# Kernel optimization log

Hardware: AMD Instinct MI355X
Metric: run time of the kernel (lower is better)

Reference implementation:

```python
import jax, jax.numpy as jnp
import numpy as np

B, L, CIN, COUT, HEADS = 8, 2048, 256, 256, 4
HD = COUT // HEADS
NEG_SLOPE = 0.2


def setup_inputs() -> dict:
    key = jax.random.key(0)
    k1, k2, k3, k4, k5 = jax.random.split(key, 5)
    x = jax.random.normal(k1, (B, L, CIN), dtype=jnp.float32)
    adj_mask = jax.random.randint(k2, (B, L, L), 0, 2) > 0  # bool [B,L,L]
    W = jax.random.normal(k3, (COUT, CIN), dtype=jnp.float32) * (1.0 / np.sqrt(CIN))
    att_src = jax.random.normal(k4, (1, HEADS, 1, HD), dtype=jnp.float32) * 0.1
    att_dst = jax.random.normal(k5, (1, HEADS, 1, HD), dtype=jnp.float32) * 0.1
    return {"x": x, "adj_mask": adj_mask, "W": W, "att_src": att_src, "att_dst": att_dst}


def reference(x, adj_mask, W, att_src, att_dst):
    Bb, Ll, _ = x.shape
    # linear projection (no bias), split heads: [B, H, L, D]
    h = jnp.einsum('blc,oc->blo', x, W).reshape(Bb, Ll, HEADS, HD).transpose(0, 2, 1, 3)
    # additive GAT scores
    a_src = jnp.sum(h * att_src, axis=-1, keepdims=True)          # [B,H,L,1]
    a_dst = jnp.sum(h * att_dst, axis=-1, keepdims=True)          # [B,H,L,1]
    e = a_src + jnp.swapaxes(a_dst, 2, 3)                          # [B,H,L,L]
    e = jnp.where(e >= 0, e, NEG_SLOPE * e)                        # leaky relu
    fill = jnp.finfo(e.dtype).min
    e = jnp.where(adj_mask[:, None, :, :], e, fill)                # mask non-edges
    alpha = jax.nn.softmax(e, axis=-1)                             # [B,H,L,L]
    # dropout is identity in eval/reference mode
    out = jnp.einsum('bhij,bhjd->bhid', alpha, h)                  # [B,H,L,D]
    return out.transpose(0, 2, 1, 3).reshape(Bb, Ll, COUT)
```

## Files before the change

### kernel.cpp

```cpp
#include <hip/hip_runtime.h>

#define B_ 8
#define L_ 2048
#define CIN_ 256
#define COUT_ 256
#define HEADS_ 4
#define HD_ 64
#define NEG_SLOPE_ 0.2f

#define TI 32
#define TJ 64

typedef __attribute__((ext_vector_type(4))) float f32x4;
typedef __attribute__((ext_vector_type(8))) __bf16 bf16x8;
typedef __attribute__((ext_vector_type(4))) __bf16 bf16x4;


__global__ __launch_bounds__(256, 2)
void proj_kernel(const float* __restrict__ x, const float* __restrict__ W,
                 const float* __restrict__ att_src, const float* __restrict__ att_dst,
                 __bf16* __restrict__ hT, float* __restrict__ a_src,
                 float* __restrict__ a_dst) {
  __shared__ __align__(16) __bf16 Wl[COUT_][80];
  __shared__ __align__(16) __bf16 Al[2][2][512];
  __shared__ __align__(16) __bf16 Tl[4][64][48];

  const int tid = threadIdx.x;
  const int r0 = blockIdx.x * TI;
  const int b  = r0 >> 11;
  const int l0 = r0 & (L_ - 1);

  const int w = tid >> 6, lane = tid & 63, col = lane & 15, q = lane >> 4;
  const int si = tid >> 3, soct = tid & 7;
  const int wn = tid >> 2, wkq = tid & 3;

  f32x4 acc[2][4];
#pragma unroll
  for (int mt = 0; mt < 2; ++mt)
#pragma unroll
    for (int nt = 0; nt < 4; ++nt) acc[mt][nt] = (f32x4)0.f;

  for (int kc = 0; kc < CIN_ / 64; ++kc) {
    __syncthreads();
#pragma unroll
    for (int rg = 0; rg < 4; ++rg) {
      const int row = rg * 64 + wn;
      const float4* ws = (const float4*)(W + (size_t)row * CIN_ + kc * 64 + wkq * 16);
#pragma unroll
      for (int u = 0; u < 4; ++u) {
        float4 f = ws[u];
        bf16x4 v;
        v[0] = (__bf16)f.x; v[1] = (__bf16)f.y; v[2] = (__bf16)f.z; v[3] = (__bf16)f.w;
        *(bf16x4*)&Wl[row][wkq * 16 + u * 4] = v;
      }
    }
    {
      const float4* xs = (const float4*)(x + (size_t)(r0 + si) * CIN_ + kc * 64 + soct * 8);
      float4 f0 = xs[0], f1 = xs[1];
      bf16x8 v;
      v[0] = (__bf16)f0.x; v[1] = (__bf16)f0.y; v[2] = (__bf16)f0.z; v[3] = (__bf16)f0.w;
      v[4] = (__bf16)f1.x; v[5] = (__bf16)f1.y; v[6] = (__bf16)f1.z; v[7] = (__bf16)f1.w;
      *(bf16x8*)&Al[si >> 4][soct >> 2][(((soct & 3) << 4) + (si & 15)) << 3] = v;
    }
    __syncthreads();

    bf16x8 af[2][2], bfr[2][4];
#pragma unroll
    for (int mt = 0; mt < 2; ++mt)
#pragma unroll
      for (int kt = 0; kt < 2; ++kt)
        af[mt][kt] = *(const bf16x8*)&Al[mt][kt][lane << 3];
#pragma unroll
    for (int kt = 0; kt < 2; ++kt)
#pragma unroll
      for (int nt = 0; nt < 4; ++nt)
        bfr[kt][nt] = *(const bf16x8*)&Wl[w * 64 + nt * 16 + col][kt * 32 + q * 8];
#pragma unroll
    for (int kt = 0; kt < 2; ++kt)
#pragma unroll
      for (int mt = 0; mt < 2; ++mt)
#pragma unroll
        for (int nt = 0; nt < 4; ++nt)
          acc[mt][nt] = __builtin_amdgcn_mfma_f32_16x16x32_bf16(
              af[mt][kt], bfr[kt][nt], acc[mt][nt], 0, 0, 0);
  }

  float asv[4], adv[4];
#pragma unroll
  for (int nt = 0; nt < 4; ++nt) {
    asv[nt] = att_src[w * 64 + nt * 16 + col];
    adv[nt] = att_dst[w * 64 + nt * 16 + col];
  }
#pragma unroll
  for (int mt = 0; mt < 2; ++mt)
#pragma unroll
    for (int reg = 0; reg < 4; ++reg) {
      float s = 0.f, d = 0.f;
#pragma unroll
      for (int nt = 0; nt < 4; ++nt) {
        s = fmaf(acc[mt][nt][reg], asv[nt], s);
        d = fmaf(acc[mt][nt][reg], adv[nt], d);
      }
      s += __shfl_xor(s, 1, 64); d += __shfl_xor(d, 1, 64);
      s += __shfl_xor(s, 2, 64); d += __shfl_xor(d, 2, 64);
      s += __shfl_xor(s, 4, 64); d += __shfl_xor(d, 4, 64);
      s += __shfl_xor(s, 8, 64); d += __shfl_xor(d, 8, 64);
      if (col == 0) {
        int il = mt * 16 + q * 4 + reg;
        a_src[((size_t)(b * HEADS_ + w) << 11) + l0 + il] = s;
        a_dst[((size_t)(b * HEADS_ + w) << 11) + l0 + il] = d;
      }
    }

#pragma unroll
  for (int mt = 0; mt < 2; ++mt)
#pragma unroll
    for (int nt = 0; nt < 4; ++nt)
#pragma unroll
      for (int reg = 0; reg < 4; ++reg)
        Tl[w][nt * 16 + col][mt * 16 + q * 4 + reg] = (__bf16)acc[mt][nt][reg];
  __syncthreads();
  {
    const size_t hrow = ((size_t)(b * COUT_ + w * 64 + lane) << 11) + l0;
#pragma unroll
    for (int u = 0; u < 4; ++u) {
      uint4 v = *(const uint4*)&Tl[w][lane][u * 8];
      *(uint4*)(hT + hrow + u * 8) = v;
    }
  }
}

__global__ __launch_bounds__(256, 2)
void attn_kernel(const __bf16* __restrict__ hT, const float* __restrict__ a_src,
                 const float* __restrict__ a_dst, const int* __restrict__ adj,
                 float* __restrict__ out) {
  __shared__ __align__(16) __bf16 Pf[HEADS_][2][2][512];
  __shared__ __align__(16) __bf16 hs[COUT_][80];
  __shared__ float l_s[HEADS_][TI];

  const int tid = threadIdx.x;
  const int b  = blockIdx.x >> 6;
  const int i0 = (blockIdx.x & 63) * TI;

  const int w = tid >> 6, lane = tid & 63, col = lane & 15, q = lane >> 4;
  const int ii1 = tid >> 3, oct = tid & 7;
  const int mtp = ii1 >> 4, ktp = oct >> 2;
  const int lanep = ((oct & 3) << 4) + (ii1 & 15);

  float asr[HEADS_];
#pragma unroll
  for (int h = 0; h < HEADS_; ++h)
    asr[h] = a_src[((size_t)(b * HEADS_ + h) << 11) + i0 + ii1];

  float lacc[HEADS_] = {0.f, 0.f, 0.f, 0.f};
  f32x4 acc[2][4];
#pragma unroll
  for (int mt = 0; mt < 2; ++mt)
#pragma unroll
    for (int nt = 0; nt < 4; ++nt) acc[mt][nt] = (f32x4)0.f;

  for (int jt = 0; jt < L_ / TJ; ++jt) {
    const int j0 = jt * TJ;
    __syncthreads();

#pragma unroll
    for (int p = 0; p < 8; ++p) {
      int c = p * 32 + (tid >> 3);
      int seg = tid & 7;
      uint4 v = *(const uint4*)(hT + (((size_t)(b * COUT_ + c)) << 11) + j0 + seg * 8);
      *(uint4*)&hs[c][seg * 8] = v;
    }

    const int4* ap =
        (const int4*)(adj + (size_t)b * L_ * L_ + (size_t)(i0 + ii1) * L_ + j0 + oct * 8);
    const int4 m0 = ap[0], m1 = ap[1];
    const int am[8] = {m0.x, m0.y, m0.z, m0.w, m1.x, m1.y, m1.z, m1.w};

#pragma unroll
    for (int h = 0; h < HEADS_; ++h) {
      const float* ad = a_dst + ((size_t)(b * HEADS_ + h) << 11) + j0 + oct * 8;
      const float4 d0 = *(const float4*)ad;
      const float4 d1 = *(const float4*)(ad + 4);
      const float dv[8] = {d0.x, d0.y, d0.z, d0.w, d1.x, d1.y, d1.z, d1.w};
      bf16x8 pv;
      float ls = 0.f;
#pragma unroll
      for (int e = 0; e < 8; ++e) {
        float s = asr[h] + dv[e];
        s = (s >= 0.f) ? s : NEG_SLOPE_ * s;
        float p = am[e] ? __expf(s) : 0.f;
        ls += p;
        pv[e] = (__bf16)p;
      }
      lacc[h] += ls;
      *(bf16x8*)&Pf[h][mtp][ktp][lanep << 3] = pv;
    }
    __syncthreads();

    bf16x8 af[2][2], bfr[2][4];
#pragma unroll
    for (int mt = 0; mt < 2; ++mt)
#pragma unroll
      for (int kt = 0; kt < 2; ++kt)
        af[mt][kt] = *(const bf16x8*)&Pf[w][mt][kt][lane << 3];
#pragma unroll
    for (int kt = 0; kt < 2; ++kt)
#pragma unroll
      for (int nt = 0; nt < 4; ++nt)
        bfr[kt][nt] = *(const bf16x8*)&hs[w * 64 + nt * 16 + col][kt * 32 + q * 8];
#pragma unroll
    for (int kt = 0; kt < 2; ++kt)
#pragma unroll
      for (int mt = 0; mt < 2; ++mt)
#pragma unroll
        for (int nt = 0; nt < 4; ++nt)
          acc[mt][nt] = __builtin_amdgcn_mfma_f32_16x16x32_bf16(
              af[mt][kt], bfr[kt][nt], acc[mt][nt], 0, 0, 0);
  }

#pragma unroll
  for (int h = 0; h < HEADS_; ++h) {
    float v = lacc[h];
    v += __shfl_xor(v, 1, 64);
    v += __shfl_xor(v, 2, 64);
    v += __shfl_xor(v, 4, 64);
    if (oct == 0) l_s[h][ii1] = v;
  }
  __syncthreads();

#pragma unroll
  for (int mt = 0; mt < 2; ++mt)
#pragma unroll
    for (int reg = 0; reg < 4; ++reg) {
      const int il = mt * 16 + q * 4 + reg;
      const float linv = 1.0f / l_s[w][il];
#pragma unroll
      for (int nt = 0; nt < 4; ++nt) {
        const int c = w * 64 + nt * 16 + col;
        out[((size_t)(b * L_ + i0 + il)) * COUT_ + c] = acc[mt][nt][reg] * linv;
      }
    }
}

extern "C" void kernel_launch(void* const* d_in, const int* in_sizes, int n_in,
                              void* d_out, int out_size, void* d_ws, size_t ws_size,
                              hipStream_t stream) {
  const float* x       = (const float*)d_in[0];
  const int*   adj     = (const int*)d_in[1];
  const float* W       = (const float*)d_in[2];
  const float* att_src = (const float*)d_in[3];
  const float* att_dst = (const float*)d_in[4];
  float* out = (float*)d_out;

  __bf16* hT   = (__bf16*)d_ws;
  float* a_src = (float*)((char*)d_ws + (size_t)B_ * COUT_ * L_ * 2);
  float* a_dst = a_src + (size_t)B_ * HEADS_ * L_;

  proj_kernel<<<(B_ * L_) / TI, 256, 0, stream>>>(x, W, att_src, att_dst, hT, a_src, a_dst);
  attn_kernel<<<B_ * (L_ / TI), 256, 0, stream>>>(hT, a_src, a_dst, adj, out);
}
```

Before: 305.8 us.

## Enlarge attention row tile, load h fragments directly, prefetch next tile

```diff
diff --git a/kernel.cpp b/kernel.cpp
--- a/kernel.cpp
+++ b/kernel.cpp
@@ -9,7 +9,9 @@
 #define NEG_SLOPE_ 0.2f
 
 #define TI 32
+#define ATI 64
 #define TJ 64
+#define NJT (L_ / TJ)
 
 typedef __attribute__((ext_vector_type(4))) float f32x4;
 typedef __attribute__((ext_vector_type(8))) __bf16 bf16x8;
@@ -130,28 +132,38 @@
   }
 }
 
-__global__ __launch_bounds__(256, 2)
+__device__ __forceinline__ int sw_chunk(int c) {
+  return c ^ (((c >> 4) & 3) << 1);
+}
+
+__global__ __launch_bounds__(512, 2)
 void attn_kernel(const __bf16* __restrict__ hT, const float* __restrict__ a_src,
                  const float* __restrict__ a_dst, const int* __restrict__ adj,
                  float* __restrict__ out) {
-  __shared__ __align__(16) __bf16 Pf[HEADS_][2][2][512];
-  __shared__ __align__(16) __bf16 hs[COUT_][80];
-  __shared__ float l_s[HEADS_][TI];
+  __shared__ __align__(16) __bf16 Pf[HEADS_][4][2][512];
+  __shared__ float l_s[HEADS_][ATI];
 
   const int tid = threadIdx.x;
-  const int b  = blockIdx.x >> 6;
-  const int i0 = (blockIdx.x & 63) * TI;
+  const int b  = blockIdx.x & 7;
+  const int i0 = (blockIdx.x >> 3) * ATI;
 
   const int w = tid >> 6, lane = tid & 63, col = lane & 15, q = lane >> 4;
+  const int hh = w >> 1;
+  const int mh = (w & 1) * 2;
   const int ii1 = tid >> 3, oct = tid & 7;
   const int mtp = ii1 >> 4, ktp = oct >> 2;
   const int lanep = ((oct & 3) << 4) + (ii1 & 15);
+  const int pchunk = sw_chunk(lanep) << 3;
 
   float asr[HEADS_];
 #pragma unroll
   for (int h = 0; h < HEADS_; ++h)
     asr[h] = a_src[((size_t)(b * HEADS_ + h) << 11) + i0 + ii1];
 
+  const int* adjrow = adj + (size_t)b * L_ * L_ + (size_t)(i0 + ii1) * L_ + oct * 8;
+  const float* adbase = a_dst + ((size_t)b * HEADS_ << 11) + oct * 8;
+  const __bf16* hbase = hT + ((size_t)(b * COUT_ + hh * 64) << 11);
+
   float lacc[HEADS_] = {0.f, 0.f, 0.f, 0.f};
   f32x4 acc[2][4];
 #pragma unroll
@@ -159,55 +171,64 @@
 #pragma unroll
     for (int nt = 0; nt < 4; ++nt) acc[mt][nt] = (f32x4)0.f;
 
-  for (int jt = 0; jt < L_ / TJ; ++jt) {
-    const int j0 = jt * TJ;
-    __syncthreads();
-
-#pragma unroll
-    for (int p = 0; p < 8; ++p) {
-      int c = p * 32 + (tid >> 3);
-      int seg = tid & 7;
-      uint4 v = *(const uint4*)(hT + (((size_t)(b * COUT_ + c)) << 11) + j0 + seg * 8);
-      *(uint4*)&hs[c][seg * 8] = v;
-    }
-
-    const int4* ap =
-        (const int4*)(adj + (size_t)b * L_ * L_ + (size_t)(i0 + ii1) * L_ + j0 + oct * 8);
-    const int4 m0 = ap[0], m1 = ap[1];
-    const int am[8] = {m0.x, m0.y, m0.z, m0.w, m1.x, m1.y, m1.z, m1.w};
-
+  int4 cadj0 = ((const int4*)adjrow)[0];
+  int4 cadj1 = ((const int4*)adjrow)[1];
+  float4 cad[HEADS_][2];
+#pragma unroll
+  for (int h = 0; h < HEADS_; ++h) {
+    cad[h][0] = *(const float4*)(adbase + ((size_t)h << 11));
+    cad[h][1] = *(const float4*)(adbase + ((size_t)h << 11) + 4);
+  }
+  bf16x8 bfr[2][4];
+#pragma unroll
+  for (int kt = 0; kt < 2; ++kt)
+#pragma unroll
+    for (int nt = 0; nt < 4; ++nt)
+      bfr[kt][nt] = *(const bf16x8*)(hbase + ((size_t)(nt * 16 + col) << 11) +
+                                     kt * 32 + q * 8);
+
+  for (int jt = 0; jt < NJT; ++jt) {
+    const int jn = (jt < NJT - 1) ? (jt + 1) * TJ : jt * TJ;
+
+    int4 nadj0 = ((const int4*)(adjrow + jn))[0];
+    int4 nadj1 = ((const int4*)(adjrow + jn))[1];
+
+    const int am[8] = {cadj0.x, cadj0.y, cadj0.z, cadj0.w,
+                       cadj1.x, cadj1.y, cadj1.z, cadj1.w};
+    bf16x8 pv[HEADS_];
 #pragma unroll
     for (int h = 0; h < HEADS_; ++h) {
-      const float* ad = a_dst + ((size_t)(b * HEADS_ + h) << 11) + j0 + oct * 8;
-      const float4 d0 = *(const float4*)ad;
-      const float4 d1 = *(const float4*)(ad + 4);
-      const float dv[8] = {d0.x, d0.y, d0.z, d0.w, d1.x, d1.y, d1.z, d1.w};
-      bf16x8 pv;
+      const float dv[8] = {cad[h][0].x, cad[h][0].y, cad[h][0].z, cad[h][0].w,
+                           cad[h][1].x, cad[h][1].y, cad[h][1].z, cad[h][1].w};
       float ls = 0.f;
 #pragma unroll
       for (int e = 0; e < 8; ++e) {
         float s = asr[h] + dv[e];
-        s = (s >= 0.f) ? s : NEG_SLOPE_ * s;
+        s = fmaxf(s, NEG_SLOPE_ * s);
         float p = am[e] ? __expf(s) : 0.f;
         ls += p;
-        pv[e] = (__bf16)p;
+        pv[h][e] = (__bf16)p;
       }
       lacc[h] += ls;
-      *(bf16x8*)&Pf[h][mtp][ktp][lanep << 3] = pv;
-    }
-    __syncthreads();
-
-    bf16x8 af[2][2], bfr[2][4];
+    }
+#pragma unroll
+    for (int h = 0; h < HEADS_; ++h) {
+      cad[h][0] = *(const float4*)(adbase + ((size_t)h << 11) + jn);
+      cad[h][1] = *(const float4*)(adbase + ((size_t)h << 11) + jn + 4);
+    }
+
+    __syncthreads();
+#pragma unroll
+    for (int h = 0; h < HEADS_; ++h)
+      *(bf16x8*)&Pf[h][mtp][ktp][pchunk] = pv[h];
+    __syncthreads();
+
+    bf16x8 af[2][2];
 #pragma unroll
     for (int mt = 0; mt < 2; ++mt)
 #pragma unroll
       for (int kt = 0; kt < 2; ++kt)
-        af[mt][kt] = *(const bf16x8*)&Pf[w][mt][kt][lane << 3];
-#pragma unroll
-    for (int kt = 0; kt < 2; ++kt)
-#pragma unroll
-      for (int nt = 0; nt < 4; ++nt)
-        bfr[kt][nt] = *(const bf16x8*)&hs[w * 64 + nt * 16 + col][kt * 32 + q * 8];
+        af[mt][kt] = *(const bf16x8*)&Pf[hh][mh + mt][kt][sw_chunk(lane) << 3];
 #pragma unroll
     for (int kt = 0; kt < 2; ++kt)
 #pragma unroll
@@ -216,6 +237,15 @@
         for (int nt = 0; nt < 4; ++nt)
           acc[mt][nt] = __builtin_amdgcn_mfma_f32_16x16x32_bf16(
               af[mt][kt], bfr[kt][nt], acc[mt][nt], 0, 0, 0);
+
+#pragma unroll
+    for (int kt = 0; kt < 2; ++kt)
+#pragma unroll
+      for (int nt = 0; nt < 4; ++nt)
+        bfr[kt][nt] = *(const bf16x8*)(hbase + ((size_t)(nt * 16 + col) << 11) +
+                                       jn + kt * 32 + q * 8);
+    cadj0 = nadj0;
+    cadj1 = nadj1;
   }
 
 #pragma unroll
@@ -232,11 +262,11 @@
   for (int mt = 0; mt < 2; ++mt)
 #pragma unroll
     for (int reg = 0; reg < 4; ++reg) {
-      const int il = mt * 16 + q * 4 + reg;
-      const float linv = 1.0f / l_s[w][il];
+      const int il = (mh + mt) * 16 + q * 4 + reg;
+      const float linv = 1.0f / l_s[hh][il];
 #pragma unroll
       for (int nt = 0; nt < 4; ++nt) {
-        const int c = w * 64 + nt * 16 + col;
+        const int c = hh * 64 + nt * 16 + col;
         out[((size_t)(b * L_ + i0 + il)) * COUT_ + c] = acc[mt][nt][reg] * linv;
       }
     }
@@ -257,5 +287,5 @@
   float* a_dst = a_src + (size_t)B_ * HEADS_ * L_;
 
   proj_kernel<<<(B_ * L_) / TI, 256, 0, stream>>>(x, W, att_src, att_dst, hT, a_src, a_dst);
-  attn_kernel<<<B_ * (L_ / TI), 256, 0, stream>>>(hT, a_src, a_dst, adj, out);
-}
+  attn_kernel<<<B_ * (L_ / ATI), 512, 0, stream>>>(hT, a_src, a_dst, adj, out);
+}
```

Result: faster. 280.6 us (-8.2%).

## Restructure attention kernel to register-direct MFMA operands without shared memory

Applied to the files above, without the earlier changes.

```diff
diff --git a/kernel.cpp b/kernel.cpp
--- a/kernel.cpp
+++ b/kernel.cpp
@@ -10,6 +10,7 @@
 
 #define TI 32
 #define TJ 64
+#define NJT (L_ / TJ)
 
 typedef __attribute__((ext_vector_type(4))) float f32x4;
 typedef __attribute__((ext_vector_type(8))) __bf16 bf16x8;
@@ -130,116 +131,102 @@
   }
 }
 
-__global__ __launch_bounds__(256, 2)
+__global__ __launch_bounds__(512, 4)
 void attn_kernel(const __bf16* __restrict__ hT, const float* __restrict__ a_src,
                  const float* __restrict__ a_dst, const int* __restrict__ adj,
                  float* __restrict__ out) {
-  __shared__ __align__(16) __bf16 Pf[HEADS_][2][2][512];
-  __shared__ __align__(16) __bf16 hs[COUT_][80];
-  __shared__ float l_s[HEADS_][TI];
-
   const int tid = threadIdx.x;
-  const int b  = blockIdx.x >> 6;
-  const int i0 = (blockIdx.x & 63) * TI;
+  const int b  = blockIdx.x & 7;
+  const int i0 = (blockIdx.x >> 3) * 32;
 
   const int w = tid >> 6, lane = tid & 63, col = lane & 15, q = lane >> 4;
-  const int ii1 = tid >> 3, oct = tid & 7;
-  const int mtp = ii1 >> 4, ktp = oct >> 2;
-  const int lanep = ((oct & 3) << 4) + (ii1 & 15);
-
-  float asr[HEADS_];
-#pragma unroll
-  for (int h = 0; h < HEADS_; ++h)
-    asr[h] = a_src[((size_t)(b * HEADS_ + h) << 11) + i0 + ii1];
-
-  float lacc[HEADS_] = {0.f, 0.f, 0.f, 0.f};
-  f32x4 acc[2][4];
-#pragma unroll
-  for (int mt = 0; mt < 2; ++mt)
-#pragma unroll
-    for (int nt = 0; nt < 4; ++nt) acc[mt][nt] = (f32x4)0.f;
-
-  for (int jt = 0; jt < L_ / TJ; ++jt) {
+  const int hh = w >> 1;
+  const int half = w & 1;
+  const int rA = i0 + half * 16 + col;
+
+  const float asr = a_src[((size_t)(b * HEADS_ + hh) << 11) + rA];
+  const int* adjrow = adj + ((size_t)b * L_ + rA) * L_ + q * 8;
+  const float* adb  = a_dst + ((size_t)(b * HEADS_ + hh) << 11) + q * 8;
+  const __bf16* hbase = hT + ((size_t)(b * COUT_ + hh * 64) << 11);
+
+  float lacc = 0.f;
+  f32x4 acc[4];
+#pragma unroll
+  for (int nt = 0; nt < 4; ++nt) acc[nt] = (f32x4)0.f;
+
+  int4 cadj[2][2];
+#pragma unroll
+  for (int kt = 0; kt < 2; ++kt) {
+    cadj[kt][0] = *(const int4*)(adjrow + kt * 32);
+    cadj[kt][1] = *(const int4*)(adjrow + kt * 32 + 4);
+  }
+
+  for (int jt = 0; jt < NJT; ++jt) {
     const int j0 = jt * TJ;
-    __syncthreads();
-
-#pragma unroll
-    for (int p = 0; p < 8; ++p) {
-      int c = p * 32 + (tid >> 3);
-      int seg = tid & 7;
-      uint4 v = *(const uint4*)(hT + (((size_t)(b * COUT_ + c)) << 11) + j0 + seg * 8);
-      *(uint4*)&hs[c][seg * 8] = v;
-    }
-
-    const int4* ap =
-        (const int4*)(adj + (size_t)b * L_ * L_ + (size_t)(i0 + ii1) * L_ + j0 + oct * 8);
-    const int4 m0 = ap[0], m1 = ap[1];
-    const int am[8] = {m0.x, m0.y, m0.z, m0.w, m1.x, m1.y, m1.z, m1.w};
-
-#pragma unroll
-    for (int h = 0; h < HEADS_; ++h) {
-      const float* ad = a_dst + ((size_t)(b * HEADS_ + h) << 11) + j0 + oct * 8;
-      const float4 d0 = *(const float4*)ad;
-      const float4 d1 = *(const float4*)(ad + 4);
-      const float dv[8] = {d0.x, d0.y, d0.z, d0.w, d1.x, d1.y, d1.z, d1.w};
-      bf16x8 pv;
-      float ls = 0.f;
+    const int jn = ((jt < NJT - 1) ? jt + 1 : jt) * TJ;
+
+    bf16x8 bfr[2][4];
+#pragma unroll
+    for (int kt = 0; kt < 2; ++kt)
+#pragma unroll
+      for (int nt = 0; nt < 4; ++nt)
+        bfr[kt][nt] = *(const bf16x8*)(hbase + ((size_t)(nt * 16 + col) << 11) +
+                                       j0 + kt * 32 + q * 8);
+    float4 dv[2][2];
+#pragma unroll
+    for (int kt = 0; kt < 2; ++kt) {
+      dv[kt][0] = *(const float4*)(adb + j0 + kt * 32);
+      dv[kt][1] = *(const float4*)(adb + j0 + kt * 32 + 4);
+    }
+    int4 nadj[2][2];
+#pragma unroll
+    for (int kt = 0; kt < 2; ++kt) {
+      nadj[kt][0] = *(const int4*)(adjrow + jn + kt * 32);
+      nadj[kt][1] = *(const int4*)(adjrow + jn + kt * 32 + 4);
+    }
+
+    bf16x8 av[2];
+#pragma unroll
+    for (int kt = 0; kt < 2; ++kt) {
+      const int am[8] = {cadj[kt][0].x, cadj[kt][0].y, cadj[kt][0].z, cadj[kt][0].w,
+                         cadj[kt][1].x, cadj[kt][1].y, cadj[kt][1].z, cadj[kt][1].w};
+      const float dd[8] = {dv[kt][0].x, dv[kt][0].y, dv[kt][0].z, dv[kt][0].w,
+                           dv[kt][1].x, dv[kt][1].y, dv[kt][1].z, dv[kt][1].w};
 #pragma unroll
       for (int e = 0; e < 8; ++e) {
-        float s = asr[h] + dv[e];
-        s = (s >= 0.f) ? s : NEG_SLOPE_ * s;
+        float s = asr + dd[e];
+        s = fmaxf(s, NEG_SLOPE_ * s);
         float p = am[e] ? __expf(s) : 0.f;
-        ls += p;
-        pv[e] = (__bf16)p;
-      }
-      lacc[h] += ls;
-      *(bf16x8*)&Pf[h][mtp][ktp][lanep << 3] = pv;
-    }
-    __syncthreads();
-
-    bf16x8 af[2][2], bfr[2][4];
-#pragma unroll
-    for (int mt = 0; mt < 2; ++mt)
-#pragma unroll
-      for (int kt = 0; kt < 2; ++kt)
-        af[mt][kt] = *(const bf16x8*)&Pf[w][mt][kt][lane << 3];
+        lacc += p;
+        av[kt][e] = (__bf16)p;
+      }
+    }
+
 #pragma unroll
     for (int kt = 0; kt < 2; ++kt)
 #pragma unroll
       for (int nt = 0; nt < 4; ++nt)
-        bfr[kt][nt] = *(const bf16x8*)&hs[w * 64 + nt * 16 + col][kt * 32 + q * 8];
-#pragma unroll
-    for (int kt = 0; kt < 2; ++kt)
-#pragma unroll
-      for (int mt = 0; mt < 2; ++mt)
-#pragma unroll
-        for (int nt = 0; nt < 4; ++nt)
-          acc[mt][nt] = __builtin_amdgcn_mfma_f32_16x16x32_bf16(
-              af[mt][kt], bfr[kt][nt], acc[mt][nt], 0, 0, 0);
-  }
-
-#pragma unroll
-  for (int h = 0; h < HEADS_; ++h) {
-    float v = lacc[h];
-    v += __shfl_xor(v, 1, 64);
-    v += __shfl_xor(v, 2, 64);
-    v += __shfl_xor(v, 4, 64);
-    if (oct == 0) l_s[h][ii1] = v;
-  }
-  __syncthreads();
-
-#pragma unroll
-  for (int mt = 0; mt < 2; ++mt)
-#pragma unroll
-    for (int reg = 0; reg < 4; ++reg) {
-      const int il = mt * 16 + q * 4 + reg;
-      const float linv = 1.0f / l_s[w][il];
-#pragma unroll
-      for (int nt = 0; nt < 4; ++nt) {
-        const int c = w * 64 + nt * 16 + col;
-        out[((size_t)(b * L_ + i0 + il)) * COUT_ + c] = acc[mt][nt][reg] * linv;
-      }
-    }
+        acc[nt] = __builtin_amdgcn_mfma_f32_16x16x32_bf16(av[kt], bfr[kt][nt],
+                                                          acc[nt], 0, 0, 0);
+#pragma unroll
+    for (int kt = 0; kt < 2; ++kt) {
+      cadj[kt][0] = nadj[kt][0];
+      cadj[kt][1] = nadj[kt][1];
+    }
+  }
+
+  lacc += __shfl_xor(lacc, 16, 64);
+  lacc += __shfl_xor(lacc, 32, 64);
+
+#pragma unroll
+  for (int reg = 0; reg < 4; ++reg) {
+    const int m = q * 4 + reg;
+    const float linv = 1.0f / __shfl(lacc, m, 64);
+    const size_t orow = ((size_t)(b * L_ + i0 + half * 16 + m)) * COUT_ + hh * 64;
+#pragma unroll
+    for (int nt = 0; nt < 4; ++nt)
+      out[orow + nt * 16 + col] = acc[nt][reg] * linv;
+  }
 }
 
 extern "C" void kernel_launch(void* const* d_in, const int* in_sizes, int n_in,
@@ -257,5 +244,5 @@
   float* a_dst = a_src + (size_t)B_ * HEADS_ * L_;
 
   proj_kernel<<<(B_ * L_) / TI, 256, 0, stream>>>(x, W, att_src, att_dst, hT, a_src, a_dst);
-  attn_kernel<<<B_ * (L_ / TI), 256, 0, stream>>>(hT, a_src, a_dst, adj, out);
+  attn_kernel<<<B_ * (L_ / 32), 512, 0, stream>>>(hT, a_src, a_dst, adj, out);
 }
```

New measurement: 368.3 us. 1.2x slower.
